# Kernel tuning notes

Measured on AMD Instinct MI355X. Metric: run time of the kernel, lower is better.

The kernel has to match this reference:

```python
import jax, jax.numpy as jnp
import numpy as np

NG = 64  # number of graphs in the batch (global_add_pool output rows)

def _bn(x, g, b):
    # BatchNorm1d, training-mode batch statistics over dim 0
    mu = x.mean(0)
    var = x.var(0)
    return (x - mu) * jax.lax.rsqrt(var + 1e-5) * g + b

def _ln(x, g, b):
    mu = x.mean(-1, keepdims=True)
    var = x.var(-1, keepdims=True)
    return (x - mu) * jax.lax.rsqrt(var + 1e-5) * g + b

def _gine(x, ei, ea, eps, w1, b1, w2, b2, n):
    # GINEConv: mlp((1+eps)*x + sum_dst ReLU(x[src] + ea))
    msg = jax.nn.relu(x[ei[0]] + ea)
    agg = jax.ops.segment_sum(msg, ei[1], num_segments=n)
    h = (1.0 + eps) * x + agg
    return jax.nn.relu(h @ w1 + b1) @ w2 + b2

def setup_inputs() -> dict:
    key = jax.random.key(0)
    H, L, RW = 128, 4, 16
    Nn, m, kk = 4096, 2, 32
    S = Nn * m; SK = S * kk
    Ei, Eg = 1048576, 65536
    Vatom, Vbond = 128, 16
    ks = jax.random.split(key, 24)
    f = lambda i, shape: jax.random.normal(ks[i], shape, jnp.float32) * 0.02
    # intra edges sampled within each subgraph block to honor locality
    subs = jax.random.randint(ks[11], (Ei,), 0, S)
    src = subs * kk + jax.random.randint(ks[12], (Ei,), 0, kk)
    dst = subs * kk + jax.random.randint(ks[13], (Ei,), 0, kk)
    inp = {
        "atom_emb": f(0, (Vatom, H)), "bond_emb": f(1, (Vbond, H)),
        "rwse_w": f(2, (RW, H)), "rwse_b": jnp.zeros((H,), jnp.float32),
        "rwse": jax.random.uniform(ks[3], (Nn, RW), jnp.float32),
        "l_eps": jnp.zeros((L,), jnp.float32),
        "l_w1": f(4, (L, H, H)), "l_b1": jnp.zeros((L, H), jnp.float32),
        "l_w2": f(5, (L, H, H)), "l_b2": jnp.zeros((L, H), jnp.float32),
        "l_bng": jnp.ones((L, H), jnp.float32), "l_bnb": jnp.zeros((L, H), jnp.float32),
        "g_eps": jnp.zeros((L,), jnp.float32),
        "g_w1": f(6, (L, H, H)), "g_b1": jnp.zeros((L, H), jnp.float32),
        "g_w2": f(7, (L, H, H)), "g_b2": jnp.zeros((L, H), jnp.float32),
        "g_bng": jnp.ones((L, H), jnp.float32), "g_bnb": jnp.zeros((L, H), jnp.float32),
        "bcast_w": f(8, (L, H, H)),
        "cat_w1": f(9, (L, 2 * H, H)), "cat_b1": jnp.zeros((L, H), jnp.float32),
        "cat_w2": f(10, (L, H, H)), "cat_b2": jnp.zeros((L, H), jnp.float32),
        "ln_g": jnp.ones((L, H), jnp.float32), "ln_b": jnp.zeros((L, H), jnp.float32),
        "x_ids": jax.random.randint(ks[14], (SK,), 0, Vatom),
        "intra_ei": jnp.stack([src, dst]),
        "intra_ea_ids": jax.random.randint(ks[15], (Ei,), 0, Vbond),
        "global_ei": jax.random.randint(ks[16], (2, Eg), 0, Nn),
        "global_ea_ids": jax.random.randint(ks[17], (Eg,), 0, Vbond),
        "node_ids": jax.random.randint(ks[18], (SK,), 0, Nn),
        "valid": jax.random.randint(ks[19], (SK,), 0, 2),
        "batch": jnp.sort(jax.random.randint(ks[20], (Nn,), 0, NG)),
        "k": 32,
    }
    return inp

def reference(atom_emb, bond_emb, rwse_w, rwse_b, rwse, l_eps, l_w1, l_b1, l_w2, l_b2, l_bng, l_bnb, g_eps, g_w1, g_b1, g_w2, g_b2, g_bng, g_bnb, bcast_w, cat_w1, cat_b1, cat_w2, cat_b2, ln_g, ln_b, x_ids, intra_ei, intra_ea_ids, global_ei, global_ea_ids, node_ids, valid, batch, k):
    SK = x_ids.shape[0]; Nn = rwse.shape[0]
    S = SK // k; m = S // Nn
    H = atom_emb.shape[1]; L = l_eps.shape[0]
    ea_flat = bond_emb[intra_ea_ids]          # [Ei, H]
    g_ea = bond_emb[global_ea_ids]            # [Eg, H]
    valid_f = valid.astype(jnp.float32)[:, None]
    h = (atom_emb[x_ids] + jax.nn.relu(rwse @ rwse_w + rwse_b)[node_ids]) * valid_f  # [SK, H]
    node_assign = jnp.repeat(jnp.arange(Nn), m)   # [S]
    root_idx = jnp.arange(S) * k                  # subgraph roots in flat layout
    for i in range(L):
        h_in = h
        h_local = _bn(jax.nn.relu(_gine(h, intra_ei, ea_flat, l_eps[i], l_w1[i], l_b1[i], l_w2[i], l_b2[i], SK)), l_bng[i], l_bnb[i])
        # scatter-mean of root reps onto original nodes (each node has exactly m subgraphs)
        h_node = jax.ops.segment_sum(h[root_idx], node_assign, num_segments=Nn) / m
        h_cross = _bn(jax.nn.relu(_gine(h_node, global_ei, g_ea, g_eps[i], g_w1[i], g_b1[i], g_w2[i], g_b2[i], Nn)), g_bng[i], g_bnb[i])
        h_node = h_node + h_cross
        # broadcast projected node reps back to every flat subgraph position
        h_b = jnp.repeat((h_node @ bcast_w[i])[node_assign], k, axis=0)  # [SK, H]
        h_cat = jnp.concatenate([h_local, h_b], axis=-1)
        h_new = _ln(jax.nn.gelu(h_cat @ cat_w1[i] + cat_b1[i], approximate=False) @ cat_w2[i] + cat_b2[i], ln_g[i], ln_b[i])
        h = (h_in + h_new) * valid_f
    # per-subgraph masked mean (h is already zero at invalid rows)
    cnt = valid_f.reshape(S, k, 1).sum(1)
    h_sub = h.reshape(S, k, H).sum(1) / jnp.maximum(cnt, 1.0)   # [S, H]
    h_nodef = h_sub.reshape(Nn, m, H).mean(1)                   # [Nn, H]
    return jax.ops.segment_sum(h_nodef, batch, num_segments=NG) # [NG, H]
```

## Files before the change

kernel.cpp:

```cpp
#include <hip/hip_runtime.h>
#include <hip/hip_bf16.h>

#define H 128
#define HH 16384
#define LNUM 4
#define NN 4096
#define SS 8192
#define SKK 262144
#define EI 1048576
#define EG 65536
#define NGRAPH 64

typedef unsigned short u16;
typedef unsigned int u32;
typedef __attribute__((ext_vector_type(8))) short s16x8;
typedef __attribute__((ext_vector_type(4))) float f32x4;

__device__ __forceinline__ float b2f(u32 u){ return __uint_as_float(u<<16); }
__device__ __forceinline__ u16 f2b(float f){
  union { __hip_bfloat16 b; u16 u; } x;
  x.b=__float2bfloat16(f);
  return x.u;
}
__device__ __forceinline__ void unp8(uint4 v, float* f){
  f[0]=b2f(v.x&0xFFFF); f[1]=b2f(v.x>>16);
  f[2]=b2f(v.y&0xFFFF); f[3]=b2f(v.y>>16);
  f[4]=b2f(v.z&0xFFFF); f[5]=b2f(v.z>>16);
  f[6]=b2f(v.w&0xFFFF); f[7]=b2f(v.w>>16);
}
__device__ __forceinline__ void unp4(uint2 v, float* f){
  f[0]=b2f(v.x&0xFFFF); f[1]=b2f(v.x>>16);
  f[2]=b2f(v.y&0xFFFF); f[3]=b2f(v.y>>16);
}
__device__ __forceinline__ uint4 pk8(const float* f){
  uint4 r;
  r.x=(u32)f2b(f[0])|((u32)f2b(f[1])<<16);
  r.y=(u32)f2b(f[2])|((u32)f2b(f[3])<<16);
  r.z=(u32)f2b(f[4])|((u32)f2b(f[5])<<16);
  r.w=(u32)f2b(f[6])|((u32)f2b(f[7])<<16);
  return r;
}
__device__ __forceinline__ uint2 pk4(const float* f){
  uint2 r;
  r.x=(u32)f2b(f[0])|((u32)f2b(f[1])<<16);
  r.y=(u32)f2b(f[2])|((u32)f2b(f[3])<<16);
  return r;
}

struct CvtArgs {
  const void* p[26];
  int start[27];
};
struct TransArgs { int src[28]; };

__global__ void k_sniff(const u16* __restrict__ a, int* __restrict__ flag){
  __shared__ int cnt;
  if(threadIdx.x==0) cnt=0;
  __syncthreads();
  int big=0;
  for(int i=threadIdx.x;i<2048;i+=256){
    int e=(a[i]>>7)&0xFF;
    if(e>=127) big++;
  }
  atomicAdd(&cnt,big);
  __syncthreads();
  if(threadIdx.x==0) *flag=(cnt<16)?1:0;
}

__global__ void k_convert(CvtArgs args, const int* __restrict__ flag, float* __restrict__ dst){
  int fl=*flag;
  int total=args.start[26];
  for(int i=blockIdx.x*blockDim.x+threadIdx.x;i<total;i+=gridDim.x*blockDim.x){
    int a=0;
    while(args.start[a+1]<=i) a++;
    int j=i-args.start[a];
    float v;
    if(fl) v=b2f(((const u16*)args.p[a])[j]);
    else   v=((const float*)args.p[a])[j];
    dst[i]=v;
  }
}

__global__ __launch_bounds__(256) void k_trans(const float* __restrict__ par, TransArgs ta, u16* __restrict__ wt){
  const float* s=par+ta.src[blockIdx.x];
  u16* d=wt+(size_t)blockIdx.x*HH;
  for(int i=threadIdx.x;i<HH;i+=256){
    int j=i&7, lane=(i>>3)&63, fc=i>>9;
    int n=fc>>2, kc=fc&3, lr=lane&15, lk=lane>>4;
    int outc=n*16+lr, k=kc*32+lk*8+j;
    d[i]=f2b(s[(size_t)k*H+outc]);
  }
}

__global__ void k_cvtbond(const float* __restrict__ b, u16* __restrict__ bb){
  int i=blockIdx.x*blockDim.x+threadIdx.x;
  if(i<16*H) bb[i]=f2b(b[i]);
}

__global__ __launch_bounds__(128) void k_prepw3(const float* __restrict__ w, const float* __restrict__ cb1,
                        const float* __restrict__ stl, const float* __restrict__ gl, const float* __restrict__ bl,
                        u16* __restrict__ wt3p, float* __restrict__ bias3){
  __shared__ float red[128];
  int c=blockIdx.x, k=threadIdx.x;
  float mu=stl[k]*(1.f/262144.f);
  float var=stl[128+k]*(1.f/262144.f)-mu*mu;
  float s=gl[k]*rsqrtf(var+1e-5f);
  float tt=bl[k]-mu*s;
  float wv=w[(size_t)k*H+c];
  int idx=(((c>>4)*4+(k>>5))*64+((k>>3)&3)*16+(c&15))*8+(k&7);
  wt3p[idx]=f2b(s*wv);
  red[k]=tt*wv;
  __syncthreads();
  for(int d=64;d>0;d>>=1){ if(k<d) red[k]+=red[k+d]; __syncthreads(); }
  if(k==0) bias3[c]=cb1[c]+red[0];
}

__global__ void k_hist(const int* __restrict__ idx, int n, int shift, int* __restrict__ cnt){
  for(int i=blockIdx.x*blockDim.x+threadIdx.x;i<n;i+=gridDim.x*blockDim.x)
    atomicAdd(&cnt[idx[i]>>shift],1);
}

__global__ void k_scan(const int* __restrict__ cnt, int* __restrict__ off, int nbins){
  __shared__ int ts[1024];
  int t=threadIdx.x;
  int per=nbins>>10;
  int base=t*per;
  int s=0;
  for(int j=0;j<per;j++) s+=cnt[base+j];
  ts[t]=s;
  __syncthreads();
  for(int d=1;d<1024;d<<=1){
    int v=(t>=d)?ts[t-d]:0;
    __syncthreads();
    ts[t]+=v;
    __syncthreads();
  }
  int ex=(t==0)?0:ts[t-1];
  for(int j=0;j<per;j++){ off[base+j]=ex; ex+=cnt[base+j]; }
}

__global__ void k_scatter_i(const int* __restrict__ ei, const int* __restrict__ ea,
                            const int* __restrict__ off, int* __restrict__ cur, int* __restrict__ pack){
  for(int i=blockIdx.x*blockDim.x+threadIdx.x;i<EI;i+=gridDim.x*blockDim.x){
    int s=ei[i], d=ei[EI+i];
    int sub=d>>5;
    int pos=off[sub]+atomicAdd(&cur[sub],1);
    pack[pos]=((s&31)<<9)|((d&31)<<4)|(ea[i]&15);
  }
}

__global__ __launch_bounds__(128) void k_sortsub(const int* __restrict__ eoff, const int* __restrict__ ecnt,
                                                 int* __restrict__ epack, int* __restrict__ dstoff){
  __shared__ int ein[512];
  __shared__ int eout[512];
  __shared__ int bcnt[32];
  __shared__ int bpos[32];
  int sub=blockIdx.x, t=threadIdx.x;
  int o=eoff[sub];
  int n=ecnt[sub]; if(n>512) n=512;
  for(int i=t;i<n;i+=128) ein[i]=epack[o+i];
  if(t<32) bcnt[t]=0;
  __syncthreads();
  for(int i=t;i<n;i+=128) atomicAdd(&bcnt[(ein[i]>>4)&31],1);
  __syncthreads();
  if(t==0){
    int s=0;
    for(int b=0;b<32;b++){ bpos[b]=s; s+=bcnt[b]; }
  }
  __syncthreads();
  if(t<32) dstoff[sub*32+t]=bpos[t];
  __syncthreads();
  for(int i=t;i<n;i+=128){
    int p=ein[i];
    int pos=atomicAdd(&bpos[(p>>4)&31],1);
    eout[pos]=p;
  }
  __syncthreads();
  for(int i=t;i<n;i+=128) epack[o+i]=eout[i];
}

__global__ void k_scatter_g(const int* __restrict__ ei, const int* __restrict__ ea,
                            const int* __restrict__ off, int* __restrict__ cur, int* __restrict__ pack){
  for(int i=blockIdx.x*blockDim.x+threadIdx.x;i<EG;i+=gridDim.x*blockDim.x){
    int s=ei[i], d=ei[EG+i];
    int pos=off[d]+atomicAdd(&cur[d],1);
    pack[pos]=(s<<4)|(ea[i]&15);
  }
}

__global__ __launch_bounds__(128) void k_rwse(const float* __restrict__ rwse, const float* __restrict__ w,
                      const float* __restrict__ b, float* __restrict__ rf){
  __shared__ float ws[16*128];
  __shared__ float rv[16];
  int n=blockIdx.x, c=threadIdx.x;
  for(int i=c;i<2048;i+=128) ws[i]=w[i];
  if(c<16) rv[c]=rwse[n*16+c];
  __syncthreads();
  float acc=b[c];
  for(int j=0;j<16;j++) acc=fmaf(rv[j],ws[j*128+c],acc);
  rf[(size_t)n*H+c]=fmaxf(acc,0.f);
}

__global__ void k_h0(const float* __restrict__ atom, const float* __restrict__ rf,
                     const int* __restrict__ xids, const int* __restrict__ nids,
                     const int* __restrict__ valid, u16* __restrict__ h){
  int i=blockIdx.x*blockDim.x+threadIdx.x;
  if(i>=SKK*16) return;
  int r=i>>4, q=i&15;
  const float4* ap=(const float4*)(atom+(size_t)xids[r]*H)+q*2;
  const float4* bp=(const float4*)(rf+(size_t)nids[r]*H)+q*2;
  float4 a0=ap[0],a1=ap[1],b0=bp[0],b1=bp[1];
  float vm=valid[r]?1.f:0.f;
  float f[8]={(a0.x+b0.x)*vm,(a0.y+b0.y)*vm,(a0.z+b0.z)*vm,(a0.w+b0.w)*vm,
              (a1.x+b1.x)*vm,(a1.y+b1.y)*vm,(a1.z+b1.z)*vm,(a1.w+b1.w)*vm};
  ((uint4*)h)[i]=pk8(f);
}

template<int TAIL>
__global__ __launch_bounds__(256) void k_fused1(
    const u16* __restrict__ h, const u16* __restrict__ beb,
    const int* __restrict__ eoff, const int* __restrict__ ecnt, const int* __restrict__ epack,
    const int* __restrict__ dstoff,
    const float* __restrict__ epsp, int layer,
    const u16* __restrict__ W1p, const float* __restrict__ b1,
    const u16* __restrict__ W2p, const float* __restrict__ b2,
    u16* __restrict__ Xg, float* __restrict__ stats,
    const u16* __restrict__ W3p, const float* __restrict__ bias3,
    const u16* __restrict__ bbv,
    const u16* __restrict__ Wc2p, const float* __restrict__ cb2,
    const float* __restrict__ lng, const float* __restrict__ lnb,
    const int* __restrict__ validv, u16* __restrict__ hio)
{
  __shared__ u16 hs[64*128];
  __shared__ u16 agx[64*128];
  __shared__ u16 bes[16*128];
  __shared__ int epk[2][512];
  __shared__ int doff[2][32];
  __shared__ float sst[256];

  int t=threadIdx.x;
  int grp=t>>7, c=t&127;
  size_t hbase=(size_t)blockIdx.x*64*H;
  int wave=t>>6, lane=t&63, lr=lane&15, lk=lane>>4;
  int rl=wave*16+lr;
  u32 rsw=((u32)(rl&7))<<4;
  int row0=blockIdx.x*64;

  {
    u32 row=(u32)(t>>4), colb=(u32)((t&15)*16);
    *(uint4*)((char*)bes+row*256+(colb^((row&7)<<4)))=((const uint4*)beb)[t];
    sst[t]=0.f;
  }
  int sub=blockIdx.x*2+grp;
  int n=min(ecnt[sub],512);
  int o=eoff[sub];
  if(c<32) doff[grp][c]=dstoff[sub*32+c];
  for(int i=c;i<n;i+=128) epk[grp][i]=epack[o+i];

  if(TAIL){
    f32x4 a1t[8];
    #pragma unroll
    for(int n8=0;n8<8;n8++) a1t[n8]=(f32x4){0.f,0.f,0.f,0.f};
    const s16x8* B0=(const s16x8*)(Xg+(size_t)(row0+rl)*H);
    #pragma unroll
    for(int kc=0;kc<4;kc++){
      s16x8 bf=B0[kc*4+lk];
      #pragma unroll
      for(int n8=0;n8<8;n8++){
        s16x8 af=*(const s16x8*)(W3p+((n8*4+kc)<<9)+lane*8);
        a1t[n8]=__builtin_amdgcn_mfma_f32_16x16x32_bf16(af,bf,a1t[n8],0,0,0);
      }
    }
    #pragma unroll
    for(int n8=0;n8<8;n8++){
      int c0=n8*16+lk*4;
      float4 b4=*(const float4*)(bias3+c0);
      float rb[4];
      unp4(*(const uint2*)(bbv+(size_t)blockIdx.x*H+c0),rb);
      float vb[4]={b4.x,b4.y,b4.z,b4.w};
      float v[4];
      #pragma unroll
      for(int j=0;j<4;j++){
        float x=a1t[n8][j]+vb[j]+rb[j];
        v[j]=0.5f*x*(1.f+erff(x*0.70710678118654752f));
      }
      *(uint2*)((char*)agx+(u32)rl*256+(((u32)(2*c0))^rsw))=pk4(v);
    }
    f32x4 a2t[8];
    #pragma unroll
    for(int n8=0;n8<8;n8++) a2t[n8]=(f32x4){0.f,0.f,0.f,0.f};
    #pragma unroll
    for(int kc=0;kc<4;kc++){
      u32 cb=(u32)((kc*32+lk*8)*2);
      s16x8 bf=*(const s16x8*)((char*)agx+(u32)rl*256+(cb^rsw));
      #pragma unroll
      for(int n8=0;n8<8;n8++){
        s16x8 af=*(const s16x8*)(Wc2p+((n8*4+kc)<<9)+lane*8);
        a2t[n8]=__builtin_amdgcn_mfma_f32_16x16x32_bf16(af,bf,a2t[n8],0,0,0);
      }
    }
    {
      float s=0.f,q=0.f;
      #pragma unroll
      for(int n8=0;n8<8;n8++){
        int c0=n8*16+lk*4;
        float4 b4=*(const float4*)(cb2+c0);
        float vb[4]={b4.x,b4.y,b4.z,b4.w};
        #pragma unroll
        for(int j=0;j<4;j++){
          float v=a2t[n8][j]+vb[j];
          a2t[n8][j]=v;
          s+=v; q+=v*v;
        }
      }
      s+=__shfl_xor(s,16); s+=__shfl_xor(s,32);
      q+=__shfl_xor(q,16); q+=__shfl_xor(q,32);
      float mu=s*(1.f/128.f);
      float rsig=rsqrtf(q*(1.f/128.f)-mu*mu+1e-5f);
      #pragma unroll
      for(int n8=0;n8<8;n8++){
        int c0=n8*16+lk*4;
        float4 g4=*(const float4*)(lng+c0);
        float4 e4=*(const float4*)(lnb+c0);
        float g[4]={g4.x,g4.y,g4.z,g4.w}, e[4]={e4.x,e4.y,e4.z,e4.w};
        float ov[4];
        #pragma unroll
        for(int j=0;j<4;j++) ov[j]=(a2t[n8][j]-mu)*rsig*g[j]+e[j];
        *(uint2*)((char*)agx+(u32)rl*256+(((u32)(2*c0))^rsw))=pk4(ov);
      }
    }
    __syncthreads();
    uint4* hp=(uint4*)(hio+hbase);
    #pragma unroll
    for(int p=0;p<4;p++){
      int i=t+p*256;
      u32 row=(u32)(i>>4), colb=(u32)((i&15)*16);
      int grow=row0+(int)row;
      uint4 v=*(const uint4*)((const char*)agx+row*256+(colb^((row&7)<<4)));
      uint4 r=hp[i];
      float vv[8],rv[8],o8[8];
      unp8(v,vv); unp8(r,rv);
      float vm=validv[grow]?1.f:0.f;
      #pragma unroll
      for(int j=0;j<8;j++) o8[j]=(rv[j]+vv[j])*vm;
      uint4 pk=pk8(o8);
      hp[i]=pk;
      *(uint4*)((char*)hs+row*256+(colb^((row&7)<<4)))=pk;
    }
  } else {
    const uint4* src=(const uint4*)(h+hbase);
    #pragma unroll
    for(int i0=0;i0<4;i0++){
      int i=t+i0*256;
      u32 row=(u32)(i>>4), colb=(u32)((i&15)*16);
      *(uint4*)((char*)hs+row*256+(colb^((row&7)<<4)))=src[i];
    }
  }
  __syncthreads();

  {
    int slot=c>>4, chg=c&15;
    u32 cbyte=(u32)chg*16;
    float ep=1.f+epsp[layer];
    #pragma unroll
    for(int k=0;k<4;k++){
      int d=slot*4+k;
      int s0=doff[grp][d];
      int s1=(d==31)?n:doff[grp][d+1];
      float acc[8]={0.f,0.f,0.f,0.f,0.f,0.f,0.f,0.f};
      if(s0<s1){
        int p=epk[grp][s0];
        u32 srow=(u32)(grp*32+(p>>9));
        u32 erow=(u32)(p&15);
        uint4 hv=*(const uint4*)((const char*)hs+srow*256+(cbyte^((srow&7)<<4)));
        uint4 bv=*(const uint4*)((const char*)bes+erow*256+(cbyte^((erow&7)<<4)));
        for(int i=s0+1;i<s1;i++){
          int p2=epk[grp][i];
          u32 srow2=(u32)(grp*32+(p2>>9));
          u32 erow2=(u32)(p2&15);
          uint4 hv2=*(const uint4*)((const char*)hs+srow2*256+(cbyte^((srow2&7)<<4)));
          uint4 bv2=*(const uint4*)((const char*)bes+erow2*256+(cbyte^((erow2&7)<<4)));
          float hf[8],bf8[8];
          unp8(hv,hf); unp8(bv,bf8);
          #pragma unroll
          for(int j=0;j<8;j++) acc[j]+=fmaxf(hf[j]+bf8[j],0.f);
          hv=hv2; bv=bv2;
        }
        float hf[8],bf8[8];
        unp8(hv,hf); unp8(bv,bf8);
        #pragma unroll
        for(int j=0;j<8;j++) acc[j]+=fmaxf(hf[j]+bf8[j],0.f);
      }
      u32 drow=(u32)(grp*32+d);
      float hf[8],o8[8];
      unp8(*(const uint4*)((const char*)hs+drow*256+(cbyte^((drow&7)<<4))),hf);
      #pragma unroll
      for(int j=0;j<8;j++) o8[j]=fmaf(ep,hf[j],acc[j]);
      *(uint4*)((char*)agx+drow*256+(cbyte^((drow&7)<<4)))=pk8(o8);
    }
  }
  __syncthreads();

  f32x4 a1[8];
  #pragma unroll
  for(int n8=0;n8<8;n8++) a1[n8]=(f32x4){0.f,0.f,0.f,0.f};
  #pragma unroll
  for(int kc=0;kc<4;kc++){
    u32 cb=(u32)((kc*32+lk*8)*2);
    s16x8 bf=*(const s16x8*)((char*)agx+(u32)rl*256+(cb^rsw));
    #pragma unroll
    for(int n8=0;n8<8;n8++){
      s16x8 af=*(const s16x8*)(W1p+((n8*4+kc)<<9)+lane*8);
      a1[n8]=__builtin_amdgcn_mfma_f32_16x16x32_bf16(af,bf,a1[n8],0,0,0);
    }
  }
  #pragma unroll
  for(int n8=0;n8<8;n8++){
    int c0=n8*16+lk*4;
    float4 b4=*(const float4*)(b1+c0);
    float v[4]={fmaxf(a1[n8][0]+b4.x,0.f),fmaxf(a1[n8][1]+b4.y,0.f),
                fmaxf(a1[n8][2]+b4.z,0.f),fmaxf(a1[n8][3]+b4.w,0.f)};
    *(uint2*)((char*)hs+(u32)rl*256+(((u32)(2*c0))^rsw))=pk4(v);
  }
  f32x4 a2[8];
  #pragma unroll
  for(int n8=0;n8<8;n8++) a2[n8]=(f32x4){0.f,0.f,0.f,0.f};
  #pragma unroll
  for(int kc=0;kc<4;kc++){
    u32 cb=(u32)((kc*32+lk*8)*2);
    s16x8 bf=*(const s16x8*)((char*)hs+(u32)rl*256+(cb^rsw));
    #pragma unroll
    for(int n8=0;n8<8;n8++){
      s16x8 af=*(const s16x8*)(W2p+((n8*4+kc)<<9)+lane*8);
      a2[n8]=__builtin_amdgcn_mfma_f32_16x16x32_bf16(af,bf,a2[n8],0,0,0);
    }
  }
  #pragma unroll
  for(int n8=0;n8<8;n8++){
    int c0=n8*16+lk*4;
    float4 b4=*(const float4*)(b2+c0);
    float v[4]={fmaxf(a2[n8][0]+b4.x,0.f),fmaxf(a2[n8][1]+b4.y,0.f),
                fmaxf(a2[n8][2]+b4.z,0.f),fmaxf(a2[n8][3]+b4.w,0.f)};
    *(uint2*)((char*)agx+(u32)rl*256+(((u32)(2*c0))^rsw))=pk4(v);
    float s[4],q[4];
    #pragma unroll
    for(int j=0;j<4;j++){ s[j]=v[j]; q[j]=v[j]*v[j]; }
    #pragma unroll
    for(int j=0;j<4;j++){
      #pragma unroll
      for(int d=1;d<16;d<<=1){
        s[j]+=__shfl_xor(s[j],d);
        q[j]+=__shfl_xor(q[j],d);
      }
    }
    if(lr==0){
      #pragma unroll
      for(int j=0;j<4;j++){
        atomicAdd(&sst[c0+j],s[j]);
        atomicAdd(&sst[128+c0+j],q[j]);
      }
    }
  }
  __syncthreads();
  uint4* out4=(uint4*)(Xg+hbase);
  #pragma unroll
  for(int p=0;p<4;p++){
    int i=t+p*256;
    u32 row=(u32)(i>>4), colb=(u32)((i&15)*16);
    out4[i]=*(const uint4*)((const char*)agx+row*256+(colb^((row&7)<<4)));
  }
  atomicAdd(&stats[t],sst[t]);
}

__global__ __launch_bounds__(256) void k_mlp2n(
    const u16* __restrict__ A, const u16* __restrict__ W1p, const float* __restrict__ b1,
    const u16* __restrict__ W2p, const float* __restrict__ b2,
    u16* __restrict__ out, float* __restrict__ stats)
{
  __shared__ u16 T[64*128];
  __shared__ float sst[256];
  int t=threadIdx.x;
  sst[t]=0.f;
  int wave=t>>6, lane=t&63, lr=lane&15, lk=lane>>4;
  int rl=wave*16+lr;
  u32 rsw=((u32)(rl&7))<<4;
  int row0=blockIdx.x*64;
  f32x4 a1[8];
  #pragma unroll
  for(int n8=0;n8<8;n8++) a1[n8]=(f32x4){0.f,0.f,0.f,0.f};
  const s16x8* B0=(const s16x8*)(A+(size_t)(row0+rl)*H);
  #pragma unroll
  for(int kc=0;kc<4;kc++){
    s16x8 bf=B0[kc*4+lk];
    #pragma unroll
    for(int n8=0;n8<8;n8++){
      s16x8 af=*(const s16x8*)(W1p+((n8*4+kc)<<9)+lane*8);
      a1[n8]=__builtin_amdgcn_mfma_f32_16x16x32_bf16(af,bf,a1[n8],0,0,0);
    }
  }
  #pragma unroll
  for(int n8=0;n8<8;n8++){
    int c0=n8*16+lk*4;
    float4 b4=*(const float4*)(b1+c0);
    float v[4]={fmaxf(a1[n8][0]+b4.x,0.f),fmaxf(a1[n8][1]+b4.y,0.f),
                fmaxf(a1[n8][2]+b4.z,0.f),fmaxf(a1[n8][3]+b4.w,0.f)};
    *(uint2*)((char*)T+(u32)rl*256+(((u32)(2*c0))^rsw))=pk4(v);
  }
  f32x4 a2[8];
  #pragma unroll
  for(int n8=0;n8<8;n8++) a2[n8]=(f32x4){0.f,0.f,0.f,0.f};
  #pragma unroll
  for(int kc=0;kc<4;kc++){
    u32 cb=(u32)((kc*32+lk*8)*2);
    s16x8 bf=*(const s16x8*)((char*)T+(u32)rl*256+(cb^rsw));
    #pragma unroll
    for(int n8=0;n8<8;n8++){
      s16x8 af=*(const s16x8*)(W2p+((n8*4+kc)<<9)+lane*8);
      a2[n8]=__builtin_amdgcn_mfma_f32_16x16x32_bf16(af,bf,a2[n8],0,0,0);
    }
  }
  #pragma unroll
  for(int n8=0;n8<8;n8++){
    int c0=n8*16+lk*4;
    float4 b4=*(const float4*)(b2+c0);
    float v[4]={fmaxf(a2[n8][0]+b4.x,0.f),fmaxf(a2[n8][1]+b4.y,0.f),
                fmaxf(a2[n8][2]+b4.z,0.f),fmaxf(a2[n8][3]+b4.w,0.f)};
    *(uint2*)((char*)T+(u32)rl*256+(((u32)(2*c0))^rsw))=pk4(v);
    float s[4],q[4];
    #pragma unroll
    for(int j=0;j<4;j++){ s[j]=v[j]; q[j]=v[j]*v[j]; }
    #pragma unroll
    for(int j=0;j<4;j++){
      #pragma unroll
      for(int d=1;d<16;d<<=1){
        s[j]+=__shfl_xor(s[j],d);
        q[j]+=__shfl_xor(q[j],d);
      }
    }
    if(lr==0){
      #pragma unroll
      for(int j=0;j<4;j++){
        atomicAdd(&sst[c0+j],s[j]);
        atomicAdd(&sst[128+c0+j],q[j]);
      }
    }
  }
  __syncthreads();
  uint4* out4=(uint4*)(out+(size_t)row0*H);
  #pragma unroll
  for(int p=0;p<4;p++){
    int i=t+p*256;
    u32 row=(u32)(i>>4), colb=(u32)((i&15)*16);
    out4[i]=*(const uint4*)((const char*)T+row*256+(colb^((row&7)<<4)));
  }
  atomicAdd(&stats[t],sst[t]);
}

__global__ __launch_bounds__(256) void k_bcast(
    const u16* __restrict__ hn, const u16* __restrict__ ag,
    const float* __restrict__ stg, const float* __restrict__ gg, const float* __restrict__ bg,
    const u16* __restrict__ Wbcp, const u16* __restrict__ Wc1p,
    u16* __restrict__ bb)
{
  __shared__ u16 T[64*128];
  __shared__ u16 T2[64*128];
  __shared__ float ssh[128], tsh[128];
  int t=threadIdx.x;
  int row0=blockIdx.x*64;
  if(t<128){
    float mu=stg[t]*(1.f/4096.f);
    float var=stg[128+t]*(1.f/4096.f)-mu*mu;
    float s=gg[t]*rsqrtf(var+1e-5f);
    ssh[t]=s; tsh[t]=bg[t]-mu*s;
  }
  __syncthreads();
  #pragma unroll
  for(int i0=0;i0<4;i0++){
    int i=t+i0*256;
    u32 row=(u32)(i>>4);
    int cb8=(i&15)*8;
    float hv[8],av[8],o8[8];
    unp8(((const uint4*)(hn+(size_t)row0*H))[i],hv);
    unp8(((const uint4*)(ag+(size_t)row0*H))[i],av);
    #pragma unroll
    for(int j=0;j<8;j++) o8[j]=hv[j]+fmaf(av[j],ssh[cb8+j],tsh[cb8+j]);
    *(uint4*)((char*)T+row*256+(((u32)(cb8*2))^((row&7)<<4)))=pk8(o8);
  }
  __syncthreads();
  int wave=t>>6, lane=t&63, lr=lane&15, lk=lane>>4;
  int rl=wave*16+lr;
  u32 rsw=((u32)(rl&7))<<4;
  f32x4 a1[8];
  #pragma unroll
  for(int n8=0;n8<8;n8++) a1[n8]=(f32x4){0.f,0.f,0.f,0.f};
  #pragma unroll
  for(int kc=0;kc<4;kc++){
    u32 cb=(u32)((kc*32+lk*8)*2);
    s16x8 bf=*(const s16x8*)((char*)T+(u32)rl*256+(cb^rsw));
    #pragma unroll
    for(int n8=0;n8<8;n8++){
      s16x8 af=*(const s16x8*)(Wbcp+((n8*4+kc)<<9)+lane*8);
      a1[n8]=__builtin_amdgcn_mfma_f32_16x16x32_bf16(af,bf,a1[n8],0,0,0);
    }
  }
  #pragma unroll
  for(int n8=0;n8<8;n8++){
    int c0=n8*16+lk*4;
    float v[4]={a1[n8][0],a1[n8][1],a1[n8][2],a1[n8][3]};
    *(uint2*)((char*)T2+(u32)rl*256+(((u32)(2*c0))^rsw))=pk4(v);
  }
  f32x4 a2[8];
  #pragma unroll
  for(int n8=0;n8<8;n8++) a2[n8]=(f32x4){0.f,0.f,0.f,0.f};
  #pragma unroll
  for(int kc=0;kc<4;kc++){
    u32 cb=(u32)((kc*32+lk*8)*2);
    s16x8 bf=*(const s16x8*)((char*)T2+(u32)rl*256+(cb^rsw));
    #pragma unroll
    for(int n8=0;n8<8;n8++){
      s16x8 af=*(const s16x8*)(Wc1p+((n8*4+kc)<<9)+lane*8);
      a2[n8]=__builtin_amdgcn_mfma_f32_16x16x32_bf16(af,bf,a2[n8],0,0,0);
    }
  }
  #pragma unroll
  for(int n8=0;n8<8;n8++){
    int c0=n8*16+lk*4;
    float v[4]={a2[n8][0],a2[n8][1],a2[n8][2],a2[n8][3]};
    *(uint2*)((char*)T+(u32)rl*256+(((u32)(2*c0))^rsw))=pk4(v);
  }
  __syncthreads();
  uint4* out4=(uint4*)(bb+(size_t)row0*H);
  #pragma unroll
  for(int p=0;p<4;p++){
    int i=t+p*256;
    u32 row=(u32)(i>>4), colb=(u32)((i&15)*16);
    out4[i]=*(const uint4*)((const char*)T+row*256+(colb^((row&7)<<4)));
  }
}

__global__ __launch_bounds__(256) void k_tail(
    const u16* __restrict__ X, const u16* __restrict__ W3p, const float* __restrict__ bias3,
    const u16* __restrict__ bb,
    const u16* __restrict__ W2p, const float* __restrict__ cb2,
    const float* __restrict__ lng, const float* __restrict__ lnb,
    const int* __restrict__ validv, u16* __restrict__ hio)
{
  __shared__ u16 T[64*128];
  int t=threadIdx.x;
  int wave=t>>6, lane=t&63, lr=lane&15, lk=lane>>4;
  int rl=wave*16+lr;
  u32 rsw=((u32)(rl&7))<<4;
  int row0=blockIdx.x*64;
  f32x4 acc[8];
  #pragma unroll
  for(int n8=0;n8<8;n8++) acc[n8]=(f32x4){0.f,0.f,0.f,0.f};
  const s16x8* B0=(const s16x8*)(X+(size_t)(row0+rl)*H);
  #pragma unroll
  for(int kc=0;kc<4;kc++){
    s16x8 bf=B0[kc*4+lk];
    #pragma unroll
    for(int n8=0;n8<8;n8++){
      s16x8 af=*(const s16x8*)(W3p+((n8*4+kc)<<9)+lane*8);
      acc[n8]=__builtin_amdgcn_mfma_f32_16x16x32_bf16(af,bf,acc[n8],0,0,0);
    }
  }
  #pragma unroll
  for(int n8=0;n8<8;n8++){
    int c0=n8*16+lk*4;
    float4 b4=*(const float4*)(bias3+c0);
    float rb[4];
    unp4(*(const uint2*)(bb+(size_t)blockIdx.x*H+c0),rb);
    float vb[4]={b4.x,b4.y,b4.z,b4.w};
    float v[4];
    #pragma unroll
    for(int j=0;j<4;j++){
      float x=acc[n8][j]+vb[j]+rb[j];
      v[j]=0.5f*x*(1.f+erff(x*0.70710678118654752f));
    }
    *(uint2*)((char*)T+(u32)rl*256+(((u32)(2*c0))^rsw))=pk4(v);
  }
  f32x4 a2[8];
  #pragma unroll
  for(int n8=0;n8<8;n8++) a2[n8]=(f32x4){0.f,0.f,0.f,0.f};
  #pragma unroll
  for(int kc=0;kc<4;kc++){
    u32 cb=(u32)((kc*32+lk*8)*2);
    s16x8 bf=*(const s16x8*)((char*)T+(u32)rl*256+(cb^rsw));
    #pragma unroll
    for(int n8=0;n8<8;n8++){
      s16x8 af=*(const s16x8*)(W2p+((n8*4+kc)<<9)+lane*8);
      a2[n8]=__builtin_amdgcn_mfma_f32_16x16x32_bf16(af,bf,a2[n8],0,0,0);
    }
  }
  {
    float s=0.f,q=0.f;
    #pragma unroll
    for(int n8=0;n8<8;n8++){
      int c0=n8*16+lk*4;
      float4 b4=*(const float4*)(cb2+c0);
      float vb[4]={b4.x,b4.y,b4.z,b4.w};
      #pragma unroll
      for(int j=0;j<4;j++){
        float v=a2[n8][j]+vb[j];
        a2[n8][j]=v;
        s+=v; q+=v*v;
      }
    }
    s+=__shfl_xor(s,16); s+=__shfl_xor(s,32);
    q+=__shfl_xor(q,16); q+=__shfl_xor(q,32);
    float mu=s*(1.f/128.f);
    float rsig=rsqrtf(q*(1.f/128.f)-mu*mu+1e-5f);
    #pragma unroll
    for(int n8=0;n8<8;n8++){
      int c0=n8*16+lk*4;
      float4 g4=*(const float4*)(lng+c0);
      float4 e4=*(const float4*)(lnb+c0);
      float g[4]={g4.x,g4.y,g4.z,g4.w}, e[4]={e4.x,e4.y,e4.z,e4.w};
      float ov[4];
      #pragma unroll
      for(int j=0;j<4;j++) ov[j]=(a2[n8][j]-mu)*rsig*g[j]+e[j];
      *(uint2*)((char*)T+(u32)rl*256+(((u32)(2*c0))^rsw))=pk4(ov);
    }
  }
  __syncthreads();
  uint4* hp=(uint4*)(hio+(size_t)row0*H);
  #pragma unroll
  for(int p=0;p<4;p++){
    int i=t+p*256;
    u32 row=(u32)(i>>4), colb=(u32)((i&15)*16);
    int grow=row0+(int)row;
    uint4 v=*(const uint4*)((const char*)T+row*256+(colb^((row&7)<<4)));
    uint4 r=hp[i];
    float vv[8],rv[8],o8[8];
    unp8(v,vv); unp8(r,rv);
    float vm=validv[grow]?1.f:0.f;
    #pragma unroll
    for(int j=0;j<8;j++) o8[j]=(rv[j]+vv[j])*vm;
    hp[i]=pk8(o8);
  }
}

__global__ void k_npool(const u16* __restrict__ h, u16* __restrict__ hn){
  int i=blockIdx.x*blockDim.x+threadIdx.x;
  if(i>=NN*16) return;
  int n=i>>4, q=i&15;
  const uint4* hp=(const uint4*)h;
  float a[8],b[8],o[8];
  unp8(hp[(size_t)n*1024+q],a);
  unp8(hp[(size_t)n*1024+512+q],b);
  #pragma unroll
  for(int e=0;e<8;e++) o[e]=(a[e]+b[e])*0.5f;
  ((uint4*)hn)[i]=pk8(o);
}

__global__ __launch_bounds__(128) void k_gagg(const u16* __restrict__ hn, const float* __restrict__ be,
                      const int* __restrict__ goff, const int* __restrict__ gcnt,
                      const int* __restrict__ gpack, const float* __restrict__ epsp, int layer,
                      u16* __restrict__ hhg){
  __shared__ float bes[16][128];
  int n=blockIdx.x, c=threadIdx.x;
  for(int i=0;i<16;i++) bes[i][c]=be[i*128+c];
  __syncthreads();
  float acc=0.f;
  int o=goff[n], e=o+gcnt[n];
  for(;o<e;o++){
    int p=gpack[o];
    acc+=fmaxf(b2f(hn[(size_t)(p>>4)*H+c])+bes[p&15][c],0.f);
  }
  hhg[(size_t)n*H+c]=f2b(fmaf(1.f+epsp[layer],b2f(hn[(size_t)n*H+c]),acc));
}

__global__ __launch_bounds__(128) void k_pool(const u16* __restrict__ h, const int* __restrict__ valid,
                      const int* __restrict__ batch, float* __restrict__ oacc){
  __shared__ float cs[2];
  int n=blockIdx.x, c=threadIdx.x;
  if(c<2){
    int s=0;
    for(int j=0;j<32;j++) s+=valid[n*64+c*32+j];
    cs[c]=fmaxf((float)s,1.f);
  }
  __syncthreads();
  size_t base=(size_t)n*64*H;
  float a0=0.f,a1=0.f;
  for(int j=0;j<32;j++){
    a0+=b2f(h[base+(size_t)j*H+c]);
    a1+=b2f(h[base+(size_t)(32+j)*H+c]);
  }
  float nodef=0.5f*(a0/cs[0]+a1/cs[1]);
  atomicAdd(&oacc[batch[n]*H+c],nodef);
}

__global__ void k_out(const float* __restrict__ acc, const int* __restrict__ flag, void* __restrict__ out){
  int i=blockIdx.x*blockDim.x+threadIdx.x;
  if(i>=NGRAPH*H) return;
  if(*flag) ((__hip_bfloat16*)out)[i]=__float2bfloat16(acc[i]);
  else ((float*)out)[i]=acc[i];
}

extern "C" void kernel_launch(void* const* d_in, const int* in_sizes, int n_in,
                              void* d_out, int out_size, void* d_ws, size_t ws_size,
                              hipStream_t stream){
  (void)n_in; (void)out_size;
  int pofs[27]; pofs[0]=0;
  for(int i=0;i<26;i++) pofs[i+1]=pofs[i]+in_sizes[i];
  int ptot=pofs[26];

  char* wsb=(char*)d_ws;
  size_t off=0;
  auto alloc=[&](size_t bytes)->char*{ char* p=wsb+off; off+=(bytes+255)&~(size_t)255; return p; };
  int*   flag =(int*)  alloc(4);
  float* par  =(float*)alloc((size_t)ptot*4);
  u16*   h    =(u16*)  alloc((size_t)SKK*H*2);
  u16*   X    =(u16*)  alloc((size_t)SKK*H*2);
  u16*   wt   =(u16*)  alloc((size_t)28*HH*2);
  u16*   wt3  =(u16*)  alloc((size_t)HH*2);
  float* bias3=(float*)alloc(H*4);
  float* rf   =(float*)alloc((size_t)NN*H*4);
  u16*   bondb=(u16*)  alloc((size_t)16*H*2);
  u16*   hn   =(u16*)  alloc((size_t)NN*H*2);
  u16*   hhg  =(u16*)  alloc((size_t)NN*H*2);
  u16*   ag   =(u16*)  alloc((size_t)NN*H*2);
  u16*   bb   =(u16*)  alloc((size_t)NN*H*2);
  int*   ecnt =(int*)  alloc(SS*4);
  int*   ecur =(int*)  alloc(SS*4);
  int*   gcnt =(int*)  alloc(NN*4);
  int*   gcur =(int*)  alloc(NN*4);
  float* stats=(float*)alloc(LNUM*512*4);
  float* oacc =(float*)alloc((size_t)NGRAPH*H*4);
  size_t zbytes=(size_t)SS*4+SS*4+NN*4+NN*4+LNUM*512*4+(size_t)NGRAPH*H*4;
  int* eoff  =(int*)alloc(SS*4);
  int* epack =(int*)alloc((size_t)EI*4);
  int* dstoff=(int*)alloc((size_t)SS*32*4);
  int* goff  =(int*)alloc(NN*4);
  int* gpack =(int*)alloc((size_t)EG*4);

  if(off>ws_size) return;

  const int* xids =(const int*)d_in[26];
  const int* iei  =(const int*)d_in[27];
  const int* iea  =(const int*)d_in[28];
  const int* gei  =(const int*)d_in[29];
  const int* gea  =(const int*)d_in[30];
  const int* nids =(const int*)d_in[31];
  const int* valid=(const int*)d_in[32];
  const int* batch=(const int*)d_in[33];

  const float* atom=par+pofs[0];
  const float* bond=par+pofs[1];
  const float* rw_w=par+pofs[2];
  const float* rw_b=par+pofs[3];
  const float* rwse=par+pofs[4];
  const float* leps=par+pofs[5];
  const float* lb1 =par+pofs[7];
  const float* lb2 =par+pofs[9];
  const float* lbng=par+pofs[10];
  const float* lbnb=par+pofs[11];
  const float* geps=par+pofs[12];
  const float* gb1 =par+pofs[14];
  const float* gb2 =par+pofs[16];
  const float* gbng=par+pofs[17];
  const float* gbnb=par+pofs[18];
  const float* cw1 =par+pofs[20];
  const float* cb1 =par+pofs[21];
  const float* cb2 =par+pofs[23];
  const float* lngp=par+pofs[24];
  const float* lnbp=par+pofs[25];

  k_sniff<<<1,256,0,stream>>>((const u16*)d_in[0], flag);
  CvtArgs ca;
  for(int i=0;i<26;i++){ ca.p[i]=d_in[i]; ca.start[i]=pofs[i]; }
  ca.start[26]=ptot;
  k_convert<<<1024,256,0,stream>>>(ca, flag, par);

  TransArgs ta;
  for(int l=0;l<LNUM;l++){
    ta.src[l*7+0]=pofs[6]+l*HH;
    ta.src[l*7+1]=pofs[8]+l*HH;
    ta.src[l*7+2]=pofs[13]+l*HH;
    ta.src[l*7+3]=pofs[15]+l*HH;
    ta.src[l*7+4]=pofs[19]+l*HH;
    ta.src[l*7+5]=pofs[20]+l*2*HH+HH;
    ta.src[l*7+6]=pofs[22]+l*HH;
  }
  k_trans<<<28,256,0,stream>>>(par, ta, wt);
  k_cvtbond<<<8,256,0,stream>>>(bond, bondb);

  (void)hipMemsetAsync(ecnt,0,zbytes,stream);

  k_hist<<<2048,256,0,stream>>>(iei+EI, EI, 5, ecnt);
  k_scan<<<1,1024,0,stream>>>(ecnt, eoff, SS);
  k_scatter_i<<<2048,256,0,stream>>>(iei, iea, eoff, ecur, epack);
  k_sortsub<<<SS,128,0,stream>>>(eoff, ecnt, epack, dstoff);
  k_hist<<<512,256,0,stream>>>(gei+EG, EG, 0, gcnt);
  k_scan<<<1,1024,0,stream>>>(gcnt, goff, NN);
  k_scatter_g<<<512,256,0,stream>>>(gei, gea, goff, gcur, gpack);

  k_rwse<<<NN,128,0,stream>>>(rwse, rw_w, rw_b, rf);
  k_h0<<<(SKK*16)/256,256,0,stream>>>(atom, rf, xids, nids, valid, h);

  for(int l=0;l<LNUM;l++){
    float* stl_l=stats+l*512;
    float* stg_l=stats+l*512+256;
    if(l==0){
      k_fused1<0><<<SS/2,256,0,stream>>>(h, bondb, eoff, ecnt, epack, dstoff, leps, l,
          wt+(size_t)(l*7+0)*HH, lb1+l*H, wt+(size_t)(l*7+1)*HH, lb2+l*H, X, stl_l,
          nullptr,nullptr,nullptr,nullptr,nullptr,nullptr,nullptr,nullptr,nullptr);
    } else {
      int pl=l-1;
      k_fused1<1><<<SS/2,256,0,stream>>>(h, bondb, eoff, ecnt, epack, dstoff, leps, l,
          wt+(size_t)(l*7+0)*HH, lb1+l*H, wt+(size_t)(l*7+1)*HH, lb2+l*H, X, stl_l,
          wt3, bias3, bb, wt+(size_t)(pl*7+6)*HH, cb2+pl*H,
          lngp+pl*H, lnbp+pl*H, valid, h);
    }
    k_npool<<<(NN*16)/256,256,0,stream>>>(h, hn);
    k_gagg<<<NN,128,0,stream>>>(hn, bond, goff, gcnt, gpack, geps, l, hhg);
    k_mlp2n<<<NN/64,256,0,stream>>>(hhg, wt+(size_t)(l*7+2)*HH, gb1+l*H,
        wt+(size_t)(l*7+3)*HH, gb2+l*H, ag, stg_l);
    k_bcast<<<NN/64,256,0,stream>>>(hn, ag, stg_l, gbng+l*H, gbnb+l*H,
        wt+(size_t)(l*7+4)*HH, wt+(size_t)(l*7+5)*HH, bb);
    k_prepw3<<<128,128,0,stream>>>(cw1+(size_t)l*2*HH, cb1+l*H, stl_l, lbng+l*H, lbnb+l*H, wt3, bias3);
  }
  {
    int l=LNUM-1;
    k_tail<<<SKK/64,256,0,stream>>>(X, wt3, bias3, bb,
        wt+(size_t)(l*7+6)*HH, cb2+l*H, lngp+l*H, lnbp+l*H, valid, h);
  }
  k_pool<<<NN,128,0,stream>>>(h, valid, batch, oacc);
  k_out<<<(NGRAPH*H+255)/256,256,0,stream>>>(oacc, flag, d_out);
}
```

Before: 1.219 ms.

## Flatten edge aggregation loop, shrink LDS, fuse final pooling into tail kernel

Rewrites the per-destination edge aggregation in k_fused1 as a single software-pipelined loop over all edges of a thread's four destinations, prefetching two edges ahead and accumulating into an agx buffer pre-initialised with (1+eps)*x. Edge packs are stored as u16, and the stats buffer now reuses that same LDS region, with launch bounds set to target more resident blocks. The final tail kernel now computes the per-subgraph masked mean and graph pooling directly instead of writing h back and launching k_pool. The costs are extra LDS passes and barriers, plus read-modify-write of bf16 partial sums, which adds rounding.

Result: faster. 1.181 ms (-3.1%).

```diff
diff --git a/kernel.cpp b/kernel.cpp
--- a/kernel.cpp
+++ b/kernel.cpp
@@ -217,7 +217,7 @@
 }
 
 template<int TAIL>
-__global__ __launch_bounds__(256) void k_fused1(
+__global__ __launch_bounds__(256,4) void k_fused1(
     const u16* __restrict__ h, const u16* __restrict__ beb,
     const int* __restrict__ eoff, const int* __restrict__ ecnt, const int* __restrict__ epack,
     const int* __restrict__ dstoff,
@@ -234,9 +234,9 @@
   __shared__ u16 hs[64*128];
   __shared__ u16 agx[64*128];
   __shared__ u16 bes[16*128];
-  __shared__ int epk[2][512];
+  __shared__ u16 epku[2][512];
   __shared__ int doff[2][32];
-  __shared__ float sst[256];
+  float* sst=(float*)&epku[0][0];
 
   int t=threadIdx.x;
   int grp=t>>7, c=t&127;
@@ -249,13 +249,12 @@
   {
     u32 row=(u32)(t>>4), colb=(u32)((t&15)*16);
     *(uint4*)((char*)bes+row*256+(colb^((row&7)<<4)))=((const uint4*)beb)[t];
-    sst[t]=0.f;
   }
   int sub=blockIdx.x*2+grp;
   int n=min(ecnt[sub],512);
   int o=eoff[sub];
   if(c<32) doff[grp][c]=dstoff[sub*32+c];
-  for(int i=c;i<n;i+=128) epk[grp][i]=epack[o+i];
+  for(int i=c;i<n;i+=128) epku[grp][i]=(u16)epack[o+i];
 
   if(TAIL){
     f32x4 a1t[8];
@@ -359,46 +358,121 @@
   __syncthreads();
 
   {
+    float ep=1.f+epsp[layer];
+    #pragma unroll
+    for(int p=0;p<4;p++){
+      int i=t+p*256;
+      u32 row=(u32)(i>>4), colb=(u32)((i&15)*16);
+      u32 off=row*256+(colb^((row&7)<<4));
+      float hf[8],o8[8];
+      unp8(*(const uint4*)((const char*)hs+off),hf);
+      #pragma unroll
+      for(int j=0;j<8;j++) o8[j]=ep*hf[j];
+      *(uint4*)((char*)agx+off)=pk8(o8);
+    }
+  }
+  __syncthreads();
+
+  {
     int slot=c>>4, chg=c&15;
     u32 cbyte=(u32)chg*16;
-    float ep=1.f+epsp[layer];
-    #pragma unroll
-    for(int k=0;k<4;k++){
-      int d=slot*4+k;
-      int s0=doff[grp][d];
-      int s1=(d==31)?n:doff[grp][d+1];
-      float acc[8]={0.f,0.f,0.f,0.f,0.f,0.f,0.f,0.f};
-      if(s0<s1){
-        int p=epk[grp][s0];
-        u32 srow=(u32)(grp*32+(p>>9));
-        u32 erow=(u32)(p&15);
-        uint4 hv=*(const uint4*)((const char*)hs+srow*256+(cbyte^((srow&7)<<4)));
-        uint4 bv=*(const uint4*)((const char*)bes+erow*256+(cbyte^((erow&7)<<4)));
-        for(int i=s0+1;i<s1;i++){
-          int p2=epk[grp][i];
-          u32 srow2=(u32)(grp*32+(p2>>9));
-          u32 erow2=(u32)(p2&15);
-          uint4 hv2=*(const uint4*)((const char*)hs+srow2*256+(cbyte^((srow2&7)<<4)));
-          uint4 bv2=*(const uint4*)((const char*)bes+erow2*256+(cbyte^((erow2&7)<<4)));
-          float hf[8],bf8[8];
-          unp8(hv,hf); unp8(bv,bf8);
+    int d0=slot*4;
+    int sA=doff[grp][d0],   eAs=doff[grp][d0+1];
+    int sB=doff[grp][d0+1], eBs=doff[grp][d0+2];
+    int sC=doff[grp][d0+2], eCs=doff[grp][d0+3];
+    int sD=doff[grp][d0+3];
+    int eDs=(d0+3==31)?n:doff[grp][d0+4];
+    int c1=eAs-sA;
+    int c2=c1+eBs-sB;
+    int c3=c2+eCs-sC;
+    int tot=c3+eDs-sD;
+    const u16* ep_=&epku[grp][0];
+    auto VIDX=[&](int j)->int{
+      return (j<c1)? sA+j : (j<c2)? sB+j-c1 : (j<c3)? sC+j-c2 : sD+j-c3;
+    };
+    auto LDP=[&](int p, uint4& hv, uint4& bv){
+      u32 srow=(u32)(grp*32+(p>>9));
+      u32 erow=(u32)(p&15);
+      hv=*(const uint4*)((const char*)hs+srow*256+(cbyte^((srow&7)<<4)));
+      bv=*(const uint4*)((const char*)bes+erow*256+(cbyte^((erow&7)<<4)));
+    };
+    int pA=0,pBv=0,pP0=0,pP1=0;
+    uint4 hvA,bvA,hvB,bvB;
+    hvA=bvA=hvB=bvB=make_uint4(0,0,0,0);
+    if(tot>0){ pA=ep_[VIDX(0)]; LDP(pA,hvA,bvA); }
+    if(tot>1){ pBv=ep_[VIDX(1)]; LDP(pBv,hvB,bvB); }
+    pP0=(tot>2)?ep_[VIDX(2)]:0;
+    pP1=(tot>3)?ep_[VIDX(3)]:0;
+    float acc[8]={0.f,0.f,0.f,0.f,0.f,0.f,0.f,0.f};
+    int cur=-1;
+    int j=0;
+    while(j<tot){
+      {
+        float hf[8],bf8[8];
+        unp8(hvA,hf); unp8(bvA,bf8);
+        int pc=pA;
+        if(j+2<tot){ pA=pP0; LDP(pA,hvA,bvA); }
+        pP0=pP1;
+        pP1=ep_[(j+4<tot)?VIDX(j+4):0];
+        int dl=(pc>>4)&31;
+        if(dl!=cur){
+          if(cur>=0){
+            u32 drow=(u32)(grp*32+cur);
+            u32 aoff=drow*256+(cbyte^((drow&7)<<4));
+            float of[8];
+            unp8(*(const uint4*)((const char*)agx+aoff),of);
+            #pragma unroll
+            for(int q=0;q<8;q++) of[q]+=acc[q];
+            *(uint4*)((char*)agx+aoff)=pk8(of);
+          }
           #pragma unroll
-          for(int j=0;j<8;j++) acc[j]+=fmaxf(hf[j]+bf8[j],0.f);
-          hv=hv2; bv=bv2;
+          for(int q=0;q<8;q++) acc[q]=0.f;
+          cur=dl;
         }
+        #pragma unroll
+        for(int q=0;q<8;q++) acc[q]+=fmaxf(hf[q]+bf8[q],0.f);
+      }
+      j++;
+      if(j>=tot) break;
+      {
         float hf[8],bf8[8];
-        unp8(hv,hf); unp8(bv,bf8);
+        unp8(hvB,hf); unp8(bvB,bf8);
+        int pc=pBv;
+        if(j+2<tot){ pBv=pP0; LDP(pBv,hvB,bvB); }
+        pP0=pP1;
+        pP1=ep_[(j+4<tot)?VIDX(j+4):0];
+        int dl=(pc>>4)&31;
+        if(dl!=cur){
+          if(cur>=0){
+            u32 drow=(u32)(grp*32+cur);
+            u32 aoff=drow*256+(cbyte^((drow&7)<<4));
+            float of[8];
+            unp8(*(const uint4*)((const char*)agx+aoff),of);
+            #pragma unroll
+            for(int q=0;q<8;q++) of[q]+=acc[q];
+            *(uint4*)((char*)agx+aoff)=pk8(of);
+          }
+          #pragma unroll
+          for(int q=0;q<8;q++) acc[q]=0.f;
+          cur=dl;
+        }
         #pragma unroll
-        for(int j=0;j<8;j++) acc[j]+=fmaxf(hf[j]+bf8[j],0.f);
-      }
-      u32 drow=(u32)(grp*32+d);
-      float hf[8],o8[8];
-      unp8(*(const uint4*)((const char*)hs+drow*256+(cbyte^((drow&7)<<4))),hf);
-      #pragma unroll
-      for(int j=0;j<8;j++) o8[j]=fmaf(ep,hf[j],acc[j]);
-      *(uint4*)((char*)agx+drow*256+(cbyte^((drow&7)<<4)))=pk8(o8);
-    }
-  }
+        for(int q=0;q<8;q++) acc[q]+=fmaxf(hf[q]+bf8[q],0.f);
+      }
+      j++;
+    }
+    if(cur>=0){
+      u32 drow=(u32)(grp*32+cur);
+      u32 aoff=drow*256+(cbyte^((drow&7)<<4));
+      float of[8];
+      unp8(*(const uint4*)((const char*)agx+aoff),of);
+      #pragma unroll
+      for(int q=0;q<8;q++) of[q]+=acc[q];
+      *(uint4*)((char*)agx+aoff)=pk8(of);
+    }
+  }
+  __syncthreads();
+  sst[t]=0.f;
   __syncthreads();
 
   f32x4 a1[8];
@@ -444,20 +518,20 @@
     *(uint2*)((char*)agx+(u32)rl*256+(((u32)(2*c0))^rsw))=pk4(v);
     float s[4],q[4];
     #pragma unroll
-    for(int j=0;j<4;j++){ s[j]=v[j]; q[j]=v[j]*v[j]; }
-    #pragma unroll
-    for(int j=0;j<4;j++){
+    for(int j2=0;j2<4;j2++){ s[j2]=v[j2]; q[j2]=v[j2]*v[j2]; }
+    #pragma unroll
+    for(int j2=0;j2<4;j2++){
       #pragma unroll
       for(int d=1;d<16;d<<=1){
-        s[j]+=__shfl_xor(s[j],d);
-        q[j]+=__shfl_xor(q[j],d);
+        s[j2]+=__shfl_xor(s[j2],d);
+        q[j2]+=__shfl_xor(q[j2],d);
       }
     }
     if(lr==0){
       #pragma unroll
-      for(int j=0;j<4;j++){
-        atomicAdd(&sst[c0+j],s[j]);
-        atomicAdd(&sst[128+c0+j],q[j]);
+      for(int j2=0;j2<4;j2++){
+        atomicAdd(&sst[c0+j2],s[j2]);
+        atomicAdd(&sst[128+c0+j2],q[j2]);
       }
     }
   }
@@ -638,14 +712,17 @@
   }
 }
 
-__global__ __launch_bounds__(256) void k_tail(
+__global__ __launch_bounds__(256) void k_tailpool(
     const u16* __restrict__ X, const u16* __restrict__ W3p, const float* __restrict__ bias3,
     const u16* __restrict__ bb,
     const u16* __restrict__ W2p, const float* __restrict__ cb2,
     const float* __restrict__ lng, const float* __restrict__ lnb,
-    const int* __restrict__ validv, u16* __restrict__ hio)
+    const int* __restrict__ validv, const u16* __restrict__ hres,
+    const int* __restrict__ batch, float* __restrict__ oacc)
 {
   __shared__ u16 T[64*128];
+  __shared__ float pbuf[256];
+  __shared__ float cntsh[2];
   int t=threadIdx.x;
   int wave=t>>6, lane=t&63, lr=lane&15, lk=lane>>4;
   int rl=wave*16+lr;
@@ -722,8 +799,15 @@
       *(uint2*)((char*)T+(u32)rl*256+(((u32)(2*c0))^rsw))=pk4(ov);
     }
   }
-  __syncthreads();
-  uint4* hp=(uint4*)(hio+(size_t)row0*H);
+  pbuf[t]=0.f;
+  if(t<2){
+    int s=0;
+    for(int j2=0;j2<32;j2++) s+=validv[row0+t*32+j2]?1:0;
+    cntsh[t]=fmaxf((float)s,1.f);
+  }
+  __syncthreads();
+  const uint4* hp=(const uint4*)(hres+(size_t)row0*H);
+  float s0[8]={0,0,0,0,0,0,0,0}, s1[8]={0,0,0,0,0,0,0,0};
   #pragma unroll
   for(int p=0;p<4;p++){
     int i=t+p*256;
@@ -731,12 +815,32 @@
     int grow=row0+(int)row;
     uint4 v=*(const uint4*)((const char*)T+row*256+(colb^((row&7)<<4)));
     uint4 r=hp[i];
-    float vv[8],rv[8],o8[8];
+    float vv[8],rv[8];
     unp8(v,vv); unp8(r,rv);
     float vm=validv[grow]?1.f:0.f;
     #pragma unroll
-    for(int j=0;j<8;j++) o8[j]=(rv[j]+vv[j])*vm;
-    hp[i]=pk8(o8);
+    for(int j2=0;j2<8;j2++){
+      float hn=(rv[j2]+vv[j2])*vm;
+      if(p<2) s0[j2]+=hn; else s1[j2]+=hn;
+    }
+  }
+  #pragma unroll
+  for(int j2=0;j2<8;j2++){
+    s0[j2]+=__shfl_xor(s0[j2],16); s0[j2]+=__shfl_xor(s0[j2],32);
+    s1[j2]+=__shfl_xor(s1[j2],16); s1[j2]+=__shfl_xor(s1[j2],32);
+  }
+  if((lane&48)==0){
+    int ch=(lane&15)*8;
+    #pragma unroll
+    for(int j2=0;j2<8;j2++){
+      atomicAdd(&pbuf[ch+j2],s0[j2]);
+      atomicAdd(&pbuf[128+ch+j2],s1[j2]);
+    }
+  }
+  __syncthreads();
+  if(t<128){
+    float nodef=0.5f*(pbuf[t]/cntsh[0]+pbuf[128+t]/cntsh[1]);
+    atomicAdd(&oacc[batch[blockIdx.x]*H+t],nodef);
   }
 }
 
@@ -768,26 +872,6 @@
     acc+=fmaxf(b2f(hn[(size_t)(p>>4)*H+c])+bes[p&15][c],0.f);
   }
   hhg[(size_t)n*H+c]=f2b(fmaf(1.f+epsp[layer],b2f(hn[(size_t)n*H+c]),acc));
-}
-
-__global__ __launch_bounds__(128) void k_pool(const u16* __restrict__ h, const int* __restrict__ valid,
-                      const int* __restrict__ batch, float* __restrict__ oacc){
-  __shared__ float cs[2];
-  int n=blockIdx.x, c=threadIdx.x;
-  if(c<2){
-    int s=0;
-    for(int j=0;j<32;j++) s+=valid[n*64+c*32+j];
-    cs[c]=fmaxf((float)s,1.f);
-  }
-  __syncthreads();
-  size_t base=(size_t)n*64*H;
-  float a0=0.f,a1=0.f;
-  for(int j=0;j<32;j++){
-    a0+=b2f(h[base+(size_t)j*H+c]);
-    a1+=b2f(h[base+(size_t)(32+j)*H+c]);
-  }
-  float nodef=0.5f*(a0/cs[0]+a1/cs[1]);
-  atomicAdd(&oacc[batch[n]*H+c],nodef);
 }
 
 __global__ void k_out(const float* __restrict__ acc, const int* __restrict__ flag, void* __restrict__ out){
@@ -922,9 +1006,8 @@
   }
   {
     int l=LNUM-1;
-    k_tail<<<SKK/64,256,0,stream>>>(X, wt3, bias3, bb,
-        wt+(size_t)(l*7+6)*HH, cb2+l*H, lngp+l*H, lnbp+l*H, valid, h);
-  }
-  k_pool<<<NN,128,0,stream>>>(h, valid, batch, oacc);
+    k_tailpool<<<SKK/64,256,0,stream>>>(X, wt3, bias3, bb,
+        wt+(size_t)(l*7+6)*HH, cb2+l*H, lngp+l*H, lnbp+l*H, valid, h, batch, oacc);
+  }
   k_out<<<(NGRAPH*H+255)/256,256,0,stream>>>(oacc, flag, d_out);
 }
```
